# Kernel tuning notes

Hardware: AMD Instinct MI355X
Metric: run time of the kernel (lower is better)

Reference implementation:

```python
import jax, jax.numpy as jnp
import numpy as np

EPS = 1e-6
NUM_HEADS = 32
HEAD_DIM = 128


def _rms_norm(x, w):
    # RMSNorm over last dim (head_dim)
    var = jnp.mean(x * x, axis=-1, keepdims=True)
    return x * jax.lax.rsqrt(var + EPS) * w


def _rotate_half(x):
    x1, x2 = jnp.split(x, 2, axis=-1)
    return jnp.concatenate([-x2, x1], axis=-1)


def _apply_rope(x, cos, sin):
    # x: [b, t, h, d]; cos/sin: [t, d] -> broadcast over batch and heads
    c = cos[None, :, None, :]
    s = sin[None, :, None, :]
    return x * c + _rotate_half(x) * s


def setup_inputs() -> dict:
    key = jax.random.key(0)
    ks = jax.random.split(key, 7)
    b, q_len, ctx_len, hidden = 4, 64, 4096, 4096
    total = ctx_len + q_len
    return {
        "hidden_states": jax.random.normal(ks[0], (b, q_len, hidden), jnp.float32),
        "target_hidden": jax.random.normal(ks[1], (b, ctx_len, hidden), jnp.float32),
        "cos": jax.random.uniform(ks[2], (total, HEAD_DIM), jnp.float32, -1.0, 1.0),
        "sin": jax.random.uniform(ks[3], (total, HEAD_DIM), jnp.float32, -1.0, 1.0),
        "Wqkv": jax.random.normal(ks[4], (hidden, 3 * hidden), jnp.float32) * 0.02,
        "Wo": jax.random.normal(ks[5], (hidden, hidden), jnp.float32) * 0.02,
        "q_norm_w": jnp.ones((HEAD_DIM,), jnp.float32),
    }


def reference(hidden_states, target_hidden, cos, sin, Wqkv, Wo, q_norm_w):
    b, q_len, hidden = hidden_states.shape
    ctx_len = target_hidden.shape[1]
    H, D = NUM_HEADS, HEAD_DIM

    # fused QKV projection; only the query slice is consumed (per source)
    qkv = jnp.einsum("bqh,hz->bqz", hidden_states, Wqkv)
    q = qkv[..., : H * D].reshape(b, q_len, H, D)

    # q_norm is applied twice in the source forward
    q = _rms_norm(_rms_norm(q, q_norm_w), q_norm_w)

    # KV built by concatenating raw target_hidden context with draft hidden states
    kv = jnp.concatenate([target_hidden, hidden_states], axis=1)  # [b, ctx+q, hidden]
    k = kv.reshape(b, ctx_len + q_len, H, D)
    v = k  # v = k view per source (rope applied only to k)

    # rotary: draft queries occupy positions ctx_len .. ctx_len+q_len-1
    q = _apply_rope(q, cos[ctx_len:], sin[ctx_len:])
    k = _apply_rope(k, cos, sin)

    # attention (full attention of draft queries over context + draft keys)
    scale = 1.0 / jnp.sqrt(jnp.asarray(D, q.dtype))
    scores = jnp.einsum("bqhd,bkhd->bhqk", q, k) * scale
    probs = jax.nn.softmax(scores, axis=-1)
    out = jnp.einsum("bhqk,bkhd->bqhd", probs, v)

    out = out.reshape(b, q_len, H * D)
    return jnp.einsum("bqh,ho->bqo", out, Wo)
```

## Files before the change

### kernel.cpp

```cpp
#include <hip/hip_runtime.h>

typedef __attribute__((ext_vector_type(8))) short bf16x8;
typedef __attribute__((ext_vector_type(4))) float f32x4;
typedef __attribute__((ext_vector_type(4))) short s16x4;

#define DEV __device__ __forceinline__

DEV short f2bf(float f) {
  union { float f; unsigned u; } v; v.f = f;
  unsigned r = v.u + 0x7fffu + ((v.u >> 16) & 1u);
  return (short)(r >> 16);
}

__global__ __launch_bounds__(256) void transpose_to_bf16(
    const float* __restrict__ in, long ld, short* __restrict__ out, int K) {
  __shared__ short tile[64][66];
  long k0 = blockIdx.x * 64L, n0 = blockIdx.y * 64L;
  int t = threadIdx.x;
  {
    int kl = t >> 4, nl4 = (t & 15) * 4;
#pragma unroll
    for (int i = 0; i < 4; i++) {
      int k = kl + i * 16;
      float4 v = *(const float4*)(in + (k0 + k) * ld + n0 + nl4);
      s16x4 w; w.x = f2bf(v.x); w.y = f2bf(v.y); w.z = f2bf(v.z); w.w = f2bf(v.w);
      *(s16x4*)&tile[k][nl4] = w;
    }
  }
  __syncthreads();
  {
    int nl = t >> 4, kl4 = (t & 15) * 4;
#pragma unroll
    for (int i = 0; i < 4; i++) {
      int n = nl + i * 16;
      s16x4 w;
      w.x = tile[kl4 + 0][n]; w.y = tile[kl4 + 1][n];
      w.z = tile[kl4 + 2][n]; w.w = tile[kl4 + 3][n];
      *(s16x4*)(out + (n0 + n) * (long)K + k0 + kl4) = w;
    }
  }
}

template <bool AF32>
__global__ __launch_bounds__(256) void gemm_bt_split(
    const void* __restrict__ Ap, const short* __restrict__ Bt,
    float* __restrict__ Cp, int M, int N, int K, int Kc) {
  __shared__ short As[8 * 544];
  __shared__ short Bs[8 * 544];
  int t = threadIdx.x;
  long m0 = blockIdx.y * 64L, n0 = blockIdx.x * 64L;
  int z = blockIdx.z;
  int lane = t & 63, quad = lane >> 4, m16 = lane & 15;
  int wave = t >> 6, wm = wave & 1, wn = wave >> 1;
  f32x4 acc[2][2] = {};
  int r = t >> 3, c = t & 7;

  int kbeg = z * Kc, kend = kbeg + Kc;
  for (int k0 = kbeg; k0 < kend; k0 += 64) {
    __syncthreads();
#pragma unroll
    for (int half = 0; half < 2; half++) {
      int rr = r + half * 32;
      int fb = (c >> 2) * 4 + (rr >> 4);
      int pos = (c & 3) * 16 + (rr & 15);
      int off = fb * 544 + pos * 8 + (pos >> 4) * 8;
      bf16x8 av;
      if (AF32) {
        const float* src = (const float*)Ap + (m0 + rr) * (long)K + k0 + c * 8;
        float4 x = *(const float4*)src;
        float4 y = *(const float4*)(src + 4);
        av[0] = f2bf(x.x); av[1] = f2bf(x.y); av[2] = f2bf(x.z); av[3] = f2bf(x.w);
        av[4] = f2bf(y.x); av[5] = f2bf(y.y); av[6] = f2bf(y.z); av[7] = f2bf(y.w);
      } else {
        av = *(const bf16x8*)((const short*)Ap + (m0 + rr) * (long)K + k0 + c * 8);
      }
      *(bf16x8*)&As[off] = av;
      *(bf16x8*)&Bs[off] = *(const bf16x8*)(Bt + (n0 + rr) * (long)K + k0 + c * 8);
    }
    __syncthreads();
#pragma unroll
    for (int s = 0; s < 2; s++) {
      int lo = lane * 8 + quad * 8;
      bf16x8 a0 = *(bf16x8*)&As[(s * 4 + wm * 2 + 0) * 544 + lo];
      bf16x8 a1 = *(bf16x8*)&As[(s * 4 + wm * 2 + 1) * 544 + lo];
      bf16x8 b0 = *(bf16x8*)&Bs[(s * 4 + wn * 2 + 0) * 544 + lo];
      bf16x8 b1 = *(bf16x8*)&Bs[(s * 4 + wn * 2 + 1) * 544 + lo];
      acc[0][0] = __builtin_amdgcn_mfma_f32_16x16x32_bf16(a0, b0, acc[0][0], 0, 0, 0);
      acc[0][1] = __builtin_amdgcn_mfma_f32_16x16x32_bf16(a0, b1, acc[0][1], 0, 0, 0);
      acc[1][0] = __builtin_amdgcn_mfma_f32_16x16x32_bf16(a1, b0, acc[1][0], 0, 0, 0);
      acc[1][1] = __builtin_amdgcn_mfma_f32_16x16x32_bf16(a1, b1, acc[1][1], 0, 0, 0);
    }
  }
  float* C = Cp + (long)z * M * N;
#pragma unroll
  for (int i = 0; i < 2; i++)
#pragma unroll
    for (int j = 0; j < 2; j++)
#pragma unroll
      for (int rg = 0; rg < 4; rg++) {
        long m = m0 + (wm * 2 + i) * 16 + quad * 4 + rg;
        long n = n0 + (wn * 2 + j) * 16 + m16;
        C[m * (long)N + n] = acc[i][j][rg];
      }
}

__global__ __launch_bounds__(256) void reduce4(
    const float* __restrict__ p, float* __restrict__ out, long n4, long stride) {
  long i = (blockIdx.x * 256L + threadIdx.x);
  if (i >= n4) return;
  float4 a = *(const float4*)(p + i * 4);
  float4 b = *(const float4*)(p + stride + i * 4);
  float4 c = *(const float4*)(p + 2 * stride + i * 4);
  float4 d = *(const float4*)(p + 3 * stride + i * 4);
  float4 r;
  r.x = a.x + b.x + c.x + d.x;
  r.y = a.y + b.y + c.y + d.y;
  r.z = a.z + b.z + c.z + d.z;
  r.w = a.w + b.w + c.w + d.w;
  *(float4*)(out + i * 4) = r;
}

__global__ __launch_bounds__(256) void q_norm_rope(
    const float* __restrict__ qtmp, const float* __restrict__ qw,
    const float* __restrict__ cosp, const float* __restrict__ sinp,
    short* __restrict__ qr) {
  int wid = blockIdx.x * 4 + (threadIdx.x >> 6);
  int lane = threadIdx.x & 63;
  int rrow = wid >> 5, h = wid & 31;
  long base = (long)rrow * 4096 + h * 128;
  const long STR = 256L * 4096;
  float x1 = qtmp[base + lane] + qtmp[STR + base + lane] +
             qtmp[2 * STR + base + lane] + qtmp[3 * STR + base + lane];
  float x2 = qtmp[base + 64 + lane] + qtmp[STR + base + 64 + lane] +
             qtmp[2 * STR + base + 64 + lane] + qtmp[3 * STR + base + 64 + lane];
  float w1 = qw[lane], w2 = qw[64 + lane];
  float ss = x1 * x1 + x2 * x2;
#pragma unroll
  for (int m = 1; m < 64; m <<= 1) ss += __shfl_xor(ss, m, 64);
  float rs = rsqrtf(ss * (1.0f / 128.0f) + 1e-6f);
  float y1 = x1 * rs * w1, y2 = x2 * rs * w2;
  float ss2 = y1 * y1 + y2 * y2;
#pragma unroll
  for (int m = 1; m < 64; m <<= 1) ss2 += __shfl_xor(ss2, m, 64);
  float rs2 = rsqrtf(ss2 * (1.0f / 128.0f) + 1e-6f);
  float z1 = y1 * rs2 * w1, z2 = y2 * rs2 * w2;
  long cpos = (long)(4096 + (rrow & 63)) * 128;
  float c1 = cosp[cpos + lane], c2 = cosp[cpos + 64 + lane];
  float s1 = sinp[cpos + lane], s2 = sinp[cpos + 64 + lane];
  const float scale = 0.08838834764831845f;
  float o1 = (z1 * c1 - z2 * s1) * scale;
  float o2 = (z2 * c2 + z1 * s2) * scale;
  qr[base + lane] = f2bf(o1);
  qr[base + 64 + lane] = f2bf(o2);
}

#define ATT_SPLIT 13
#define ATT_LKV 320
#define ATT_TILES 5

__global__ __launch_bounds__(256) void attn_kernel(
    const short* __restrict__ qr, const float* __restrict__ th,
    const float* __restrict__ hs, const float* __restrict__ cosp,
    const float* __restrict__ sinp, float* __restrict__ part,
    float* __restrict__ mstat, float* __restrict__ lstat) {
  __shared__ short Ks[64 * 136];
  __shared__ short Vt[128 * 80];
  __shared__ short Ps[64 * 72];
  int bh = blockIdx.x, split = blockIdx.y;
  int b = bh >> 5, h = bh & 31;
  int t = threadIdx.x;
  int wave = t >> 6, lane = t & 63, quad = lane >> 4, m16 = lane & 15;

  bf16x8 aq[4];
  {
    const short* qrow = qr + (long)(b * 64 + wave * 16 + m16) * 4096 + h * 128;
#pragma unroll
    for (int s = 0; s < 4; s++) aq[s] = *(const bf16x8*)(qrow + s * 32 + quad * 8);
  }
  float mi[4] = {-INFINITY, -INFINITY, -INFINITY, -INFINITY};
  float li[4] = {0.f, 0.f, 0.f, 0.f};
  f32x4 oacc[8] = {};

  int srow = t >> 2;
  int sc = t & 3;

  for (int tile = 0; tile < ATT_TILES; tile++) {
    int l0 = split * ATT_LKV + tile * 64;
    __syncthreads();
    {
      int lg = l0 + srow;
      const float* kvrow = (lg < 4096)
          ? th + ((long)b * 4096 + lg) * 4096 + h * 128
          : hs + ((long)b * 64 + (lg - 4096)) * 4096 + h * 128;
      const float* crow = cosp + (long)lg * 128;
      const float* srw = sinp + (long)lg * 128;
#pragma unroll
      for (int i = 0; i < 2; i++) {
        int c = sc + 4 * i;
        int d1 = c * 8, d2 = d1 + 64;
        alignas(16) float xa[8], xb[8], cA[8], sA[8], cB[8], sB[8];
        *(float4*)&xa[0] = *(const float4*)(kvrow + d1);
        *(float4*)&xa[4] = *(const float4*)(kvrow + d1 + 4);
        *(float4*)&xb[0] = *(const float4*)(kvrow + d2);
        *(float4*)&xb[4] = *(const float4*)(kvrow + d2 + 4);
        *(float4*)&cA[0] = *(const float4*)(crow + d1);
        *(float4*)&cA[4] = *(const float4*)(crow + d1 + 4);
        *(float4*)&cB[0] = *(const float4*)(crow + d2);
        *(float4*)&cB[4] = *(const float4*)(crow + d2 + 4);
        *(float4*)&sA[0] = *(const float4*)(srw + d1);
        *(float4*)&sA[4] = *(const float4*)(srw + d1 + 4);
        *(float4*)&sB[0] = *(const float4*)(srw + d2);
        *(float4*)&sB[4] = *(const float4*)(srw + d2 + 4);
        bf16x8 k1, k2, v1, v2;
#pragma unroll
        for (int j = 0; j < 8; j++) {
          k1[j] = f2bf(xa[j] * cA[j] - xb[j] * sA[j]);
          k2[j] = f2bf(xb[j] * cB[j] + xa[j] * sB[j]);
          v1[j] = f2bf(xa[j]);
          v2[j] = f2bf(xb[j]);
        }
        *(bf16x8*)&Ks[srow * 136 + d1] = k1;
        *(bf16x8*)&Ks[srow * 136 + d2] = k2;
#pragma unroll
        for (int j = 0; j < 8; j++) {
          Vt[(d1 + j) * 80 + srow] = v1[j];
          Vt[(d2 + j) * 80 + srow] = v2[j];
        }
      }
    }
    __syncthreads();

    f32x4 sacc[4] = {};
#pragma unroll
    for (int s = 0; s < 4; s++)
#pragma unroll
      for (int nt = 0; nt < 4; nt++) {
        bf16x8 bk = *(const bf16x8*)&Ks[(nt * 16 + m16) * 136 + s * 32 + quad * 8];
        sacc[nt] = __builtin_amdgcn_mfma_f32_16x16x32_bf16(aq[s], bk, sacc[nt], 0, 0, 0);
      }

    float mnew[4], alpha[4];
#pragma unroll
    for (int rg = 0; rg < 4; rg++) {
      float mx = fmaxf(fmaxf(sacc[0][rg], sacc[1][rg]), fmaxf(sacc[2][rg], sacc[3][rg]));
#pragma unroll
      for (int msk = 1; msk < 16; msk <<= 1) mx = fmaxf(mx, __shfl_xor(mx, msk, 16));
      mnew[rg] = fmaxf(mi[rg], mx);
      alpha[rg] = __expf(mi[rg] - mnew[rg]);
      mi[rg] = mnew[rg];
    }
#pragma unroll
    for (int rg = 0; rg < 4; rg++) {
      float rs = 0.f;
#pragma unroll
      for (int nt = 0; nt < 4; nt++) {
        float p = __expf(sacc[nt][rg] - mnew[rg]);
        rs += p;
        Ps[(wave * 16 + quad * 4 + rg) * 72 + nt * 16 + m16] = f2bf(p);
      }
#pragma unroll
      for (int msk = 1; msk < 16; msk <<= 1) rs += __shfl_xor(rs, msk, 16);
      li[rg] = li[rg] * alpha[rg] + rs;
    }
#pragma unroll
    for (int nt = 0; nt < 8; nt++) {
      f32x4 o = oacc[nt];
      o[0] *= alpha[0]; o[1] *= alpha[1]; o[2] *= alpha[2]; o[3] *= alpha[3];
      oacc[nt] = o;
    }

    bf16x8 ap[2];
#pragma unroll
    for (int s = 0; s < 2; s++)
      ap[s] = *(const bf16x8*)&Ps[(wave * 16 + m16) * 72 + s * 32 + quad * 8];
#pragma unroll
    for (int s = 0; s < 2; s++)
#pragma unroll
      for (int nt = 0; nt < 8; nt++) {
        bf16x8 bv = *(const bf16x8*)&Vt[(nt * 16 + m16) * 80 + s * 32 + quad * 8];
        oacc[nt] = __builtin_amdgcn_mfma_f32_16x16x32_bf16(ap[s], bv, oacc[nt], 0, 0, 0);
      }
  }

  long pbase = (long)(bh * ATT_SPLIT + split) * 64;
#pragma unroll
  for (int nt = 0; nt < 8; nt++)
#pragma unroll
    for (int rg = 0; rg < 4; rg++)
      part[(pbase + wave * 16 + quad * 4 + rg) * 128 + nt * 16 + m16] = oacc[nt][rg];
  if (m16 == 0)
#pragma unroll
    for (int rg = 0; rg < 4; rg++) {
      mstat[pbase + wave * 16 + quad * 4 + rg] = mi[rg];
      lstat[pbase + wave * 16 + quad * 4 + rg] = li[rg];
    }
}

__global__ __launch_bounds__(128) void attn_merge(
    const float* __restrict__ part, const float* __restrict__ mstat,
    const float* __restrict__ lstat, short* __restrict__ attn) {
  int idx = blockIdx.x;
  int bh = idx >> 6, q = idx & 63;
  int d = threadIdx.x;
  float mstar = -INFINITY;
#pragma unroll
  for (int s = 0; s < ATT_SPLIT; s++)
    mstar = fmaxf(mstar, mstat[((long)bh * ATT_SPLIT + s) * 64 + q]);
  float denom = 0.f, o = 0.f;
#pragma unroll
  for (int s = 0; s < ATT_SPLIT; s++) {
    long sq = ((long)bh * ATT_SPLIT + s) * 64 + q;
    float w = __expf(mstat[sq] - mstar);
    denom += w * lstat[sq];
    o += w * part[sq * 128 + d];
  }
  int b = bh >> 5, h = bh & 31;
  attn[(long)(b * 64 + q) * 4096 + h * 128 + d] = f2bf(o / denom);
}

extern "C" void kernel_launch(void* const* d_in, const int* in_sizes, int n_in,
                              void* d_out, int out_size, void* d_ws, size_t ws_size,
                              hipStream_t stream) {
  const float* hs = (const float*)d_in[0];
  const float* th = (const float*)d_in[1];
  const float* cosp = (const float*)d_in[2];
  const float* sinp = (const float*)d_in[3];
  const float* wqkv = (const float*)d_in[4];
  const float* wo = (const float*)d_in[5];
  const float* qw = (const float*)d_in[6];
  float* out = (float*)d_out;

  char* ws = (char*)d_ws;
  short* WT = (short*)ws;
  float* qtmp = (float*)(ws + (32L << 20));
  short* qrb = (short*)(ws + (48L << 20));
  short* attn = (short*)(ws + (50L << 20));
  float* part = (float*)(ws + (52L << 20));
  float* mstat = (float*)(ws + (108L << 20));
  float* lstat = (float*)(ws + (109L << 20));
  float* otmp = (float*)(ws + (110L << 20));

  transpose_to_bf16<<<dim3(64, 64), 256, 0, stream>>>(wqkv, 12288, WT, 4096);
  gemm_bt_split<true><<<dim3(64, 4, 4), 256, 0, stream>>>(hs, WT, qtmp, 256, 4096, 4096, 1024);
  q_norm_rope<<<2048, 256, 0, stream>>>(qtmp, qw, cosp, sinp, qrb);
  attn_kernel<<<dim3(128, ATT_SPLIT), 256, 0, stream>>>(qrb, th, hs, cosp, sinp,
                                                        part, mstat, lstat);
  attn_merge<<<128 * 64, 128, 0, stream>>>(part, mstat, lstat, attn);
  transpose_to_bf16<<<dim3(64, 64), 256, 0, stream>>>(wo, 4096, WT, 4096);
  gemm_bt_split<false><<<dim3(64, 4, 4), 256, 0, stream>>>(attn, WT, otmp, 256, 4096, 4096, 1024);
  reduce4<<<1024, 256, 0, stream>>>(otmp, out, 262144, 1L << 20);
}
```

Measured before the change: 636.1 us.

## Replace split-K GEMM with LDS-DMA full-M tiles, packed bf16 converts, swizzled V

Replaces the 64x64 split-K GEMM with a 512-thread kernel that covers all 256 rows per block, stages tiles with global_load_lds, and raises the split-K factor to 8. The hidden states are now pre-cast to bf16 in a separate kernel. Float-to-bf16 conversion uses the packed hardware convert where it is available, and the attention V-transpose stores and loads are XOR-swizzled to cut LDS bank conflicts. In exchange there are more partial sums to reduce and an extra cast launch.

After: 635.4 us. No clear change (-0.1%).

```diff
diff --git a/kernel.cpp b/kernel.cpp
--- a/kernel.cpp
+++ b/kernel.cpp
@@ -10,6 +10,25 @@
   union { float f; unsigned u; } v; v.f = f;
   unsigned r = v.u + 0x7fffu + ((v.u >> 16) & 1u);
   return (short)(r >> 16);
+}
+
+DEV int pk2(float a, float b) {
+#if defined(__has_builtin) && __has_builtin(__builtin_amdgcn_cvt_pk_bf16_f32)
+  auto v = __builtin_amdgcn_cvt_pk_bf16_f32(a, b);
+  int r; __builtin_memcpy(&r, &v, 4); return r;
+#else
+  return (int)(unsigned short)f2bf(a) | ((int)(unsigned short)f2bf(b) << 16);
+#endif
+}
+
+DEV void stage16(const short* g, short* lbase, int lane) {
+#if defined(__has_builtin) && __has_builtin(__builtin_amdgcn_global_load_lds)
+  (void)lane;
+  __builtin_amdgcn_global_load_lds((const __attribute__((address_space(1))) void*)g,
+                                   (__attribute__((address_space(3))) void*)lbase, 16, 0, 0);
+#else
+  *(bf16x8*)(lbase + lane * 8) = *(const bf16x8*)g;
+#endif
 }
 
 __global__ __launch_bounds__(256) void transpose_to_bf16(
@@ -23,8 +42,9 @@
     for (int i = 0; i < 4; i++) {
       int k = kl + i * 16;
       float4 v = *(const float4*)(in + (k0 + k) * ld + n0 + nl4);
-      s16x4 w; w.x = f2bf(v.x); w.y = f2bf(v.y); w.z = f2bf(v.z); w.w = f2bf(v.w);
-      *(s16x4*)&tile[k][nl4] = w;
+      int* dst = (int*)&tile[k][nl4];
+      dst[0] = pk2(v.x, v.y);
+      dst[1] = pk2(v.z, v.w);
     }
   }
   __syncthreads();
@@ -41,82 +61,82 @@
   }
 }
 
-template <bool AF32>
-__global__ __launch_bounds__(256) void gemm_bt_split(
-    const void* __restrict__ Ap, const short* __restrict__ Bt,
-    float* __restrict__ Cp, int M, int N, int K, int Kc) {
-  __shared__ short As[8 * 544];
-  __shared__ short Bs[8 * 544];
+__global__ __launch_bounds__(256) void cast_f32_bf16(
+    const float* __restrict__ in, short* __restrict__ out, int n8) {
+  int i = blockIdx.x * 256 + threadIdx.x;
+  if (i >= n8) return;
+  float4 a = *(const float4*)(in + (long)i * 8);
+  float4 b = *(const float4*)(in + (long)i * 8 + 4);
+  union { bf16x8 v; int w[4]; } r;
+  r.w[0] = pk2(a.x, a.y); r.w[1] = pk2(a.z, a.w);
+  r.w[2] = pk2(b.x, b.y); r.w[3] = pk2(b.z, b.w);
+  *(bf16x8*)(out + (long)i * 8) = r.v;
+}
+
+__global__ __launch_bounds__(512) void gemm_dma(
+    const short* __restrict__ A, const short* __restrict__ Bt,
+    float* __restrict__ Cp, int N, int K, int Kc) {
+  __shared__ short As[32 * 512];
+  __shared__ short Bs[8 * 512];
   int t = threadIdx.x;
-  long m0 = blockIdx.y * 64L, n0 = blockIdx.x * 64L;
-  int z = blockIdx.z;
-  int lane = t & 63, quad = lane >> 4, m16 = lane & 15;
-  int wave = t >> 6, wm = wave & 1, wn = wave >> 1;
-  f32x4 acc[2][2] = {};
-  int r = t >> 3, c = t & 7;
-
+  int lane = t & 63, wave = t >> 6;
+  int quad = lane >> 4, m16 = lane & 15;
+  long n0 = blockIdx.x * 64L;
+  int z = blockIdx.y;
+  f32x4 acc[2][4] = {};
   int kbeg = z * Kc, kend = kbeg + Kc;
+
   for (int k0 = kbeg; k0 < kend; k0 += 64) {
     __syncthreads();
 #pragma unroll
-    for (int half = 0; half < 2; half++) {
-      int rr = r + half * 32;
-      int fb = (c >> 2) * 4 + (rr >> 4);
-      int pos = (c & 3) * 16 + (rr & 15);
-      int off = fb * 544 + pos * 8 + (pos >> 4) * 8;
-      bf16x8 av;
-      if (AF32) {
-        const float* src = (const float*)Ap + (m0 + rr) * (long)K + k0 + c * 8;
-        float4 x = *(const float4*)src;
-        float4 y = *(const float4*)(src + 4);
-        av[0] = f2bf(x.x); av[1] = f2bf(x.y); av[2] = f2bf(x.z); av[3] = f2bf(x.w);
-        av[4] = f2bf(y.x); av[5] = f2bf(y.y); av[6] = f2bf(y.z); av[7] = f2bf(y.w);
-      } else {
-        av = *(const bf16x8*)((const short*)Ap + (m0 + rr) * (long)K + k0 + c * 8);
-      }
-      *(bf16x8*)&As[off] = av;
-      *(bf16x8*)&Bs[off] = *(const bf16x8*)(Bt + (n0 + rr) * (long)K + k0 + c * 8);
+    for (int i = 0; i < 2; i++)
+#pragma unroll
+      for (int s = 0; s < 2; s++) {
+        int row = (2 * wave + i) * 16 + m16;
+        const short* g = A + (long)row * K + k0 + (s * 4 + quad) * 8;
+        stage16(g, &As[(4 * wave + 2 * i + s) * 512], lane);
+      }
+    {
+      int nt = wave >> 1, s = wave & 1;
+      long row = n0 + nt * 16 + m16;
+      const short* g = Bt + row * (long)K + k0 + (s * 4 + quad) * 8;
+      stage16(g, &Bs[wave * 512], lane);
     }
     __syncthreads();
 #pragma unroll
     for (int s = 0; s < 2; s++) {
-      int lo = lane * 8 + quad * 8;
-      bf16x8 a0 = *(bf16x8*)&As[(s * 4 + wm * 2 + 0) * 544 + lo];
-      bf16x8 a1 = *(bf16x8*)&As[(s * 4 + wm * 2 + 1) * 544 + lo];
-      bf16x8 b0 = *(bf16x8*)&Bs[(s * 4 + wn * 2 + 0) * 544 + lo];
-      bf16x8 b1 = *(bf16x8*)&Bs[(s * 4 + wn * 2 + 1) * 544 + lo];
-      acc[0][0] = __builtin_amdgcn_mfma_f32_16x16x32_bf16(a0, b0, acc[0][0], 0, 0, 0);
-      acc[0][1] = __builtin_amdgcn_mfma_f32_16x16x32_bf16(a0, b1, acc[0][1], 0, 0, 0);
-      acc[1][0] = __builtin_amdgcn_mfma_f32_16x16x32_bf16(a1, b0, acc[1][0], 0, 0, 0);
-      acc[1][1] = __builtin_amdgcn_mfma_f32_16x16x32_bf16(a1, b1, acc[1][1], 0, 0, 0);
-    }
-  }
-  float* C = Cp + (long)z * M * N;
+      bf16x8 a0 = *(bf16x8*)&As[(4 * wave + s) * 512 + lane * 8];
+      bf16x8 a1 = *(bf16x8*)&As[(4 * wave + 2 + s) * 512 + lane * 8];
+#pragma unroll
+      for (int nt = 0; nt < 4; nt++) {
+        bf16x8 b = *(bf16x8*)&Bs[(nt * 2 + s) * 512 + lane * 8];
+        acc[0][nt] = __builtin_amdgcn_mfma_f32_16x16x32_bf16(a0, b, acc[0][nt], 0, 0, 0);
+        acc[1][nt] = __builtin_amdgcn_mfma_f32_16x16x32_bf16(a1, b, acc[1][nt], 0, 0, 0);
+      }
+    }
+  }
+  float* C = Cp + (long)z * 256 * N;
 #pragma unroll
   for (int i = 0; i < 2; i++)
 #pragma unroll
-    for (int j = 0; j < 2; j++)
+    for (int nt = 0; nt < 4; nt++)
 #pragma unroll
       for (int rg = 0; rg < 4; rg++) {
-        long m = m0 + (wm * 2 + i) * 16 + quad * 4 + rg;
-        long n = n0 + (wn * 2 + j) * 16 + m16;
-        C[m * (long)N + n] = acc[i][j][rg];
-      }
-}
-
-__global__ __launch_bounds__(256) void reduce4(
+        long m = (2 * wave + i) * 16 + quad * 4 + rg;
+        C[m * (long)N + n0 + nt * 16 + m16] = acc[i][nt][rg];
+      }
+}
+
+__global__ __launch_bounds__(256) void reduce8(
     const float* __restrict__ p, float* __restrict__ out, long n4, long stride) {
   long i = (blockIdx.x * 256L + threadIdx.x);
   if (i >= n4) return;
-  float4 a = *(const float4*)(p + i * 4);
-  float4 b = *(const float4*)(p + stride + i * 4);
-  float4 c = *(const float4*)(p + 2 * stride + i * 4);
-  float4 d = *(const float4*)(p + 3 * stride + i * 4);
-  float4 r;
-  r.x = a.x + b.x + c.x + d.x;
-  r.y = a.y + b.y + c.y + d.y;
-  r.z = a.z + b.z + c.z + d.z;
-  r.w = a.w + b.w + c.w + d.w;
+  float4 r = *(const float4*)(p + i * 4);
+#pragma unroll
+  for (int z = 1; z < 8; z++) {
+    float4 a = *(const float4*)(p + z * stride + i * 4);
+    r.x += a.x; r.y += a.y; r.z += a.z; r.w += a.w;
+  }
   *(float4*)(out + i * 4) = r;
 }
 
@@ -129,10 +149,12 @@
   int rrow = wid >> 5, h = wid & 31;
   long base = (long)rrow * 4096 + h * 128;
   const long STR = 256L * 4096;
-  float x1 = qtmp[base + lane] + qtmp[STR + base + lane] +
-             qtmp[2 * STR + base + lane] + qtmp[3 * STR + base + lane];
-  float x2 = qtmp[base + 64 + lane] + qtmp[STR + base + 64 + lane] +
-             qtmp[2 * STR + base + 64 + lane] + qtmp[3 * STR + base + 64 + lane];
+  float x1 = 0.f, x2 = 0.f;
+#pragma unroll
+  for (int z = 0; z < 8; z++) {
+    x1 += qtmp[z * STR + base + lane];
+    x2 += qtmp[z * STR + base + 64 + lane];
+  }
   float w1 = qw[lane], w2 = qw[64 + lane];
   float ss = x1 * x1 + x2 * x2;
 #pragma unroll
@@ -183,6 +205,7 @@
 
   int srow = t >> 2;
   int sc = t & 3;
+  int colw = srow ^ (sc * 16);
 
   for (int tile = 0; tile < ATT_TILES; tile++) {
     int l0 = split * ATT_LKV + tile * 64;
@@ -211,20 +234,25 @@
         *(float4*)&sA[4] = *(const float4*)(srw + d1 + 4);
         *(float4*)&sB[0] = *(const float4*)(srw + d2);
         *(float4*)&sB[4] = *(const float4*)(srw + d2 + 4);
-        bf16x8 k1, k2, v1, v2;
-#pragma unroll
-        for (int j = 0; j < 8; j++) {
-          k1[j] = f2bf(xa[j] * cA[j] - xb[j] * sA[j]);
-          k2[j] = f2bf(xb[j] * cB[j] + xa[j] * sB[j]);
-          v1[j] = f2bf(xa[j]);
-          v2[j] = f2bf(xb[j]);
+        union { bf16x8 v; int w[4]; } K1, K2;
+#pragma unroll
+        for (int jj = 0; jj < 4; jj++) {
+          int j0 = 2 * jj, j1 = 2 * jj + 1;
+          K1.w[jj] = pk2(xa[j0] * cA[j0] - xb[j0] * sA[j0],
+                         xa[j1] * cA[j1] - xb[j1] * sA[j1]);
+          K2.w[jj] = pk2(xb[j0] * cB[j0] + xa[j0] * sB[j0],
+                         xb[j1] * cB[j1] + xa[j1] * sB[j1]);
         }
-        *(bf16x8*)&Ks[srow * 136 + d1] = k1;
-        *(bf16x8*)&Ks[srow * 136 + d2] = k2;
-#pragma unroll
-        for (int j = 0; j < 8; j++) {
-          Vt[(d1 + j) * 80 + srow] = v1[j];
-          Vt[(d2 + j) * 80 + srow] = v2[j];
+        *(bf16x8*)&Ks[srow * 136 + d1] = K1.v;
+        *(bf16x8*)&Ks[srow * 136 + d2] = K2.v;
+#pragma unroll
+        for (int jj = 0; jj < 4; jj++) {
+          int p1 = pk2(xa[2 * jj], xa[2 * jj + 1]);
+          int p2 = pk2(xb[2 * jj], xb[2 * jj + 1]);
+          Vt[(d1 + 2 * jj) * 80 + colw] = (short)(p1 & 0xffff);
+          Vt[(d1 + 2 * jj + 1) * 80 + colw] = (short)((unsigned)p1 >> 16);
+          Vt[(d2 + 2 * jj) * 80 + colw] = (short)(p2 & 0xffff);
+          Vt[(d2 + 2 * jj + 1) * 80 + colw] = (short)((unsigned)p2 >> 16);
         }
       }
     }
@@ -277,7 +305,10 @@
     for (int s = 0; s < 2; s++)
 #pragma unroll
       for (int nt = 0; nt < 8; nt++) {
-        bf16x8 bv = *(const bf16x8*)&Vt[(nt * 16 + m16) * 80 + s * 32 + quad * 8];
+        int d16 = nt * 16 + m16;
+        int scd = (d16 >> 3) & 3;
+        int cb = (s * 32 + quad * 8) ^ (scd * 16);
+        bf16x8 bv = *(const bf16x8*)&Vt[d16 * 80 + cb];
         oacc[nt] = __builtin_amdgcn_mfma_f32_16x16x32_bf16(ap[s], bv, oacc[nt], 0, 0, 0);
       }
   }
@@ -331,22 +362,24 @@
   float* out = (float*)d_out;
 
   char* ws = (char*)d_ws;
-  short* WT = (short*)ws;
-  float* qtmp = (float*)(ws + (32L << 20));
-  short* qrb = (short*)(ws + (48L << 20));
-  short* attn = (short*)(ws + (50L << 20));
-  float* part = (float*)(ws + (52L << 20));
-  float* mstat = (float*)(ws + (108L << 20));
-  float* lstat = (float*)(ws + (109L << 20));
-  float* otmp = (float*)(ws + (110L << 20));
+  short* WT   = (short*)ws;
+  short* hsb  = (short*)(ws + (32L << 20));
+  float* qtmp = (float*)(ws + (34L << 20));
+  short* qrb  = (short*)(ws + (66L << 20));
+  short* attnb= (short*)(ws + (68L << 20));
+  float* part = (float*)(ws + (70L << 20));
+  float* mstat= (float*)(ws + (125L << 20));
+  float* lstat= (float*)(ws + (126L << 20));
+  float* otmp = (float*)(ws + (127L << 20));
 
   transpose_to_bf16<<<dim3(64, 64), 256, 0, stream>>>(wqkv, 12288, WT, 4096);
-  gemm_bt_split<true><<<dim3(64, 4, 4), 256, 0, stream>>>(hs, WT, qtmp, 256, 4096, 4096, 1024);
+  cast_f32_bf16<<<512, 256, 0, stream>>>(hs, hsb, 131072);
+  gemm_dma<<<dim3(64, 8), 512, 0, stream>>>(hsb, WT, qtmp, 4096, 4096, 512);
   q_norm_rope<<<2048, 256, 0, stream>>>(qtmp, qw, cosp, sinp, qrb);
   attn_kernel<<<dim3(128, ATT_SPLIT), 256, 0, stream>>>(qrb, th, hs, cosp, sinp,
                                                         part, mstat, lstat);
-  attn_merge<<<128 * 64, 128, 0, stream>>>(part, mstat, lstat, attn);
+  attn_merge<<<128 * 64, 128, 0, stream>>>(part, mstat, lstat, attnb);
   transpose_to_bf16<<<dim3(64, 64), 256, 0, stream>>>(wo, 4096, WT, 4096);
-  gemm_bt_split<false><<<dim3(64, 4, 4), 256, 0, stream>>>(attn, WT, otmp, 256, 4096, 4096, 1024);
-  reduce4<<<1024, 256, 0, stream>>>(otmp, out, 262144, 1L << 20);
-}
+  gemm_dma<<<dim3(64, 8), 512, 0, stream>>>(attnb, WT, otmp, 4096, 4096, 512);
+  reduce8<<<1024, 256, 0, stream>>>(otmp, out, 262144, 1048576);
+}
```
